# Kernel optimization log

Measured on AMD Instinct MI355X. Metric: run time of the kernel, lower is better.

The kernel has to match this reference:

```python
import jax, jax.numpy as jnp
import numpy as np
from jax import lax

B, C_IN, T = 128, 9, 2048
HID, OUT = 128, 6
NEW_T = T // 4          # two MaxPool1d(2)
N = B * NEW_T           # 65536 graph nodes
E = 524288              # edges
FEAT = 32               # out-channels of 2nd conv


def setup_inputs() -> dict:
    key = jax.random.key(0)
    ks = jax.random.split(key, 13)
    def w(k, shape, fan_in):
        return (jax.random.normal(k, shape, jnp.float32) / np.sqrt(fan_in)).astype(jnp.float32)
    return {
        "x": jax.random.normal(ks[0], (B, C_IN, T), jnp.float32),
        "edge_index": jax.random.randint(ks[1], (2, E), 0, N, jnp.int32),
        "conv1_w": w(ks[2], (16, C_IN, 5), C_IN * 5),
        "conv1_b": jnp.zeros((16,), jnp.float32),
        "conv2_w": w(ks[3], (FEAT, 16, 5), 16 * 5),
        "conv2_b": jnp.zeros((FEAT,), jnp.float32),
        "gcn1_w": w(ks[4], (FEAT, HID), FEAT),
        "gcn1_b": jnp.zeros((HID,), jnp.float32),
        "gcn2_w": w(ks[5], (HID, HID), HID),
        "gcn2_b": jnp.zeros((HID,), jnp.float32),
        "cls_w": w(ks[6], (HID, OUT), HID),
        "cls_b": jnp.zeros((OUT,), jnp.float32),
    }


def _conv1d(x, w, b):
    # x: [B, C, T], w: [O, I, K] (OIH), 'same' padding for k=5
    y = lax.conv_general_dilated(x, w, window_strides=(1,), padding=[(2, 2)],
                                 dimension_numbers=("NCH", "OIH", "NCH"))
    return y + b[None, :, None]


def _maxpool2(x):
    return lax.reduce_window(x, -jnp.inf, lax.max, (1, 1, 2), (1, 1, 2), "VALID")


def _gcn(x, w, b, src, dst, deg_inv_sqrt):
    # PyG GCNConv: sym-normalized aggregation with self loops.
    xw = x @ w                                             # [N, F]
    norm = deg_inv_sqrt[src] * deg_inv_sqrt[dst]           # [E]
    msg = xw[src] * norm[:, None]                          # gather + scale
    agg = jax.ops.segment_sum(msg, dst, num_segments=N)    # scatter-add
    agg = agg + xw * (deg_inv_sqrt * deg_inv_sqrt)[:, None]  # self loops
    return agg + b


def reference(x, edge_index, conv1_w, conv1_b, conv2_w, conv2_b,
              gcn1_w, gcn1_b, gcn2_w, gcn2_b, cls_w, cls_b):
    # temporal conv stack
    h = _maxpool2(jax.nn.relu(_conv1d(x, conv1_w, conv1_b)))
    h = _maxpool2(jax.nn.relu(_conv1d(h, conv2_w, conv2_b)))   # [B, 32, NEW_T]
    nodes = jnp.transpose(h, (0, 2, 1)).reshape(-1, FEAT)       # [N, 32]

    src, dst = edge_index[0], edge_index[1]
    # degree at dst, +1 for self loop
    deg = jax.ops.segment_sum(jnp.ones((E,), jnp.float32), dst, num_segments=N) + 1.0
    deg_inv_sqrt = lax.rsqrt(deg)

    g = jax.nn.relu(_gcn(nodes, gcn1_w, gcn1_b, src, dst, deg_inv_sqrt))
    g = jax.nn.relu(_gcn(g, gcn2_w, gcn2_b, src, dst, deg_inv_sqrt))

    pooled = g.reshape(B, NEW_T, HID).mean(axis=1)              # [B, HID]
    return pooled @ cls_w + cls_b                               # [B, OUT]
```

## Files before the change

kernel.cpp:

```cpp
#include <hip/hip_runtime.h>
#include <hip/hip_bf16.h>

#define BB    128
#define C_IN  9
#define T0    2048
#define T1    1024
#define T2    512
#define NN    65536
#define EE    524288
#define FEAT  32
#define HID   128
#define OUTC  6
#define CAP   64

typedef __attribute__((ext_vector_type(8))) short bf16x8;
typedef __attribute__((ext_vector_type(4))) float f32x4;

__device__ __forceinline__ float bf_lo(unsigned u) { return __uint_as_float(u << 16); }
__device__ __forceinline__ float bf_hi(unsigned u) { return __uint_as_float(u & 0xffff0000u); }
__device__ __forceinline__ unsigned short f2bf(float f) {
    unsigned x = __float_as_uint(f);
    return (unsigned short)((x + 0x7fffu + ((x >> 16) & 1u)) >> 16);
}
__device__ __forceinline__ float disv(int deg) { return rsqrtf((float)deg + 1.0f); }

__global__ __launch_bounds__(256) void k_zw(int4* __restrict__ cnt4,
                                            const float* __restrict__ w2,
                                            unsigned short* __restrict__ wt2) {
    int gid = blockIdx.x * 256 + threadIdx.x;
    cnt4[gid] = make_int4(0, 0, 0, 0);
    int col = gid & 127, k = gid >> 7;
    wt2[col * 128 + k] = f2bf(w2[(size_t)k * 128 + col]);
}

__global__ __launch_bounds__(256) void k_fillB(const int* __restrict__ ei,
                                               int* __restrict__ cnt,
                                               int* __restrict__ bucket) {
    int e = blockIdx.x * 256 + threadIdx.x;
    if (e >= EE) return;
    int s = ei[e];
    int d = ei[EE + e];
    int pos = atomicAdd(&cnt[d], 1);
    if (pos < CAP) bucket[d * CAP + pos] = s;
}

__global__ __launch_bounds__(256) void k_conv12(const float* __restrict__ x,
                                                const float* __restrict__ w1c,
                                                const float* __restrict__ b1c,
                                                const float* __restrict__ w2c,
                                                const float* __restrict__ b2c,
                                                const int* __restrict__ cnt,
                                                unsigned short* __restrict__ nodes_b) {
    __shared__ float sx[C_IN][272];
    __shared__ float sh[16][136];
    __shared__ float swt1[45 * 16];
    __shared__ float swt2[80 * 32];
    int b   = blockIdx.x >> 3;
    int qt  = blockIdx.x & 7;
    int tid = threadIdx.x;
    int t1lo = qt * 128 - 2;
    int gxb  = 2 * t1lo - 2;

    const float* xb = x + (size_t)b * C_IN * T0;
    #pragma unroll
    for (int c = 0; c < C_IN; ++c)
        for (int i = tid; i < 268; i += 256) {
            int g = gxb + i;
            sx[c][i] = ((unsigned)g < T0) ? xb[c * T0 + g] : 0.f;
        }
    for (int idx = tid; idx < 720; idx += 256) {
        int o = idx & 15, ck = idx >> 4;
        swt1[ck * 16 + o] = w1c[o * 45 + ck];
    }
    for (int idx = tid; idx < 2560; idx += 256) {
        int o = idx & 31, ck = idx >> 5;
        swt2[ck * 32 + o] = w2c[o * 80 + ck];
    }
    __syncthreads();

    {
        int o = tid >> 4, sub = tid & 15;
        float A0[9], A1[9];
        #pragma unroll
        for (int ii = 0; ii < 9; ++ii) { A0[ii] = 0.f; A1[ii] = 0.f; }
        #pragma unroll
        for (int c = 0; c < C_IN; ++c) {
            float wt[5];
            #pragma unroll
            for (int k = 0; k < 5; ++k) wt[k] = swt1[(c * 5 + k) * 16 + o];
            #pragma unroll
            for (int ii = 0; ii < 9; ++ii) {
                int pos = sub + ii * 16;
                if (pos < 132) {
                    const float* sp = &sx[c][2 * pos];
                    float2 p0 = *(const float2*)(sp);
                    float2 p1 = *(const float2*)(sp + 2);
                    float2 p2 = *(const float2*)(sp + 4);
                    A0[ii] += wt[0]*p0.x + wt[1]*p0.y + wt[2]*p1.x + wt[3]*p1.y + wt[4]*p2.x;
                    A1[ii] += wt[0]*p0.y + wt[1]*p1.x + wt[2]*p1.y + wt[3]*p2.x + wt[4]*p2.y;
                }
            }
        }
        float bo = b1c[o];
        #pragma unroll
        for (int ii = 0; ii < 9; ++ii) {
            int pos = sub + ii * 16;
            if (pos < 132) {
                int t = t1lo + pos;
                float h = fmaxf(fmaxf(A0[ii], A1[ii]) + bo, 0.f);
                sh[o][pos] = ((unsigned)t < T1) ? h : 0.f;
            }
        }
    }
    __syncthreads();

    int lane = tid & 63;
    int wv   = tid >> 6;
    int o    = lane & 31;
    int slot = lane >> 5;
    int ttl0 = wv * 16 + slot * 8;

    float acc[16];
    #pragma unroll
    for (int i = 0; i < 16; ++i) acc[i] = 0.f;

    #pragma unroll
    for (int c = 0; c < 16; ++c) {
        float wt[5];
        #pragma unroll
        for (int k = 0; k < 5; ++k) wt[k] = swt2[(c * 5 + k) * 32 + o];
        #pragma unroll
        for (int cb = 0; cb < 2; ++cb) {
            int Pb = 2 * ttl0 + 8 * cb;
            float4 i0 = *(const float4*)&sh[c][Pb];
            float4 i1 = *(const float4*)&sh[c][Pb + 4];
            float4 i2 = *(const float4*)&sh[c][Pb + 8];
            float in[12] = {i0.x,i0.y,i0.z,i0.w, i1.x,i1.y,i1.z,i1.w, i2.x,i2.y,i2.z,i2.w};
            #pragma unroll
            for (int q = 0; q < 8; ++q) {
                float s = acc[cb * 8 + q];
                #pragma unroll
                for (int k = 0; k < 5; ++k) s += wt[k] * in[q + k];
                acc[cb * 8 + q] = s;
            }
        }
    }

    float bi = b2c[o];
    int node0 = b * T2 + qt * 64 + ttl0;
    size_t nbase = (size_t)node0 * FEAT + o;
    #pragma unroll
    for (int cb = 0; cb < 2; ++cb)
        #pragma unroll
        for (int jj = 0; jj < 4; ++jj) {
            int node = node0 + cb * 4 + jj;
            float v = fmaxf(fmaxf(acc[cb*8+2*jj], acc[cb*8+2*jj+1]) + bi, 0.f);
            nodes_b[nbase + (size_t)(cb * 4 + jj) * FEAT] = f2bf(v * disv(cnt[node]));
        }
}

__global__ __launch_bounds__(256) void k_gather1(const unsigned short* __restrict__ nodes_b,
                                                 const int* __restrict__ cnt,
                                                 const int* __restrict__ bucket,
                                                 float* __restrict__ aggN) {
    int t = blockIdx.x * 256 + threadIdx.x;
    int node = t >> 3;
    if (node >= NN) return;
    int lane = t & 7;
    int deg = cnt[node];
    const int* bk = bucket + node * CAP;
    const uint2* nb = (const uint2*)nodes_b;
    uint2 q = nb[(size_t)node * 8 + lane];
    float a0 = bf_lo(q.x), a1 = bf_hi(q.x), a2 = bf_lo(q.y), a3 = bf_hi(q.y);
    for (int j = 0; j < deg; ++j) {
        int s = bk[j];
        uint2 p = nb[(size_t)s * 8 + lane];
        a0 += bf_lo(p.x); a1 += bf_hi(p.x); a2 += bf_lo(p.y); a3 += bf_hi(p.y);
    }
    float dd = disv(deg);
    float4 r; r.x = a0 * dd; r.y = a1 * dd; r.z = a2 * dd; r.w = a3 * dd;
    ((float4*)aggN)[(size_t)node * 8 + lane] = r;
}

__global__ __launch_bounds__(256) void k_fused(const float* __restrict__ aggN,
                                               const float* __restrict__ w1,
                                               const unsigned short* __restrict__ wt2,
                                               const float* __restrict__ b1,
                                               const int* __restrict__ cnt,
                                               unsigned short* __restrict__ xws2) {
    __shared__ union {
        struct { float an[32][132]; float w1s[32][132]; } p1;
        short sa[128 * 128];
    } u;
    __shared__ short sW[128 * 128];

    int tid = threadIdx.x;
    int rowBase = blockIdx.x * 128;

    #pragma unroll
    for (int it = 0; it < 8; ++it) {
        int cr = it * 16 + (tid >> 4);
        int ck = tid & 15;
        uint4 v = *(const uint4*)(wt2 + cr * 128 + ck * 8);
        *(uint4*)&sW[cr * 128 + ((ck * 8) ^ ((cr & 7) << 3))] = v;
    }
    {
        int ar = tid & 127;
        int half = tid >> 7;
        const float* arow = aggN + (size_t)(rowBase + ar) * FEAT + half * 16;
        #pragma unroll
        for (int q = 0; q < 4; ++q) {
            float4 va = *(const float4*)(arow + q * 4);
            int kb = half * 16 + q * 4;
            u.p1.an[kb + 0][ar] = va.x;
            u.p1.an[kb + 1][ar] = va.y;
            u.p1.an[kb + 2][ar] = va.z;
            u.p1.an[kb + 3][ar] = va.w;
        }
        #pragma unroll
        for (int it = 0; it < 4; ++it) {
            int i = tid + it * 256;
            int k  = i >> 5;
            int c4 = (i & 31) * 4;
            *(float4*)&u.p1.w1s[k][c4] = *(const float4*)(w1 + k * HID + c4);
        }
    }
    __syncthreads();

    int tr = tid >> 4, tc = tid & 15;
    float acc[8][8];
    #pragma unroll
    for (int i = 0; i < 8; ++i)
        #pragma unroll
        for (int j = 0; j < 8; ++j) acc[i][j] = 0.f;

    #pragma unroll 8
    for (int k = 0; k < FEAT; ++k) {
        float4 a0 = *(const float4*)&u.p1.an[k][tr * 8];
        float4 a1 = *(const float4*)&u.p1.an[k][tr * 8 + 4];
        float4 b0 = *(const float4*)&u.p1.w1s[k][tc * 8];
        float4 b1v = *(const float4*)&u.p1.w1s[k][tc * 8 + 4];
        float av[8] = {a0.x, a0.y, a0.z, a0.w, a1.x, a1.y, a1.z, a1.w};
        float bv[8] = {b0.x, b0.y, b0.z, b0.w, b1v.x, b1v.y, b1v.z, b1v.w};
        #pragma unroll
        for (int i = 0; i < 8; ++i)
            #pragma unroll
            for (int j = 0; j < 8; ++j) acc[i][j] += av[i] * bv[j];
    }
    __syncthreads();

    {
        float4 bb0 = *(const float4*)(b1 + tc * 8);
        float4 bb1 = *(const float4*)(b1 + tc * 8 + 4);
        float bv[8] = {bb0.x, bb0.y, bb0.z, bb0.w, bb1.x, bb1.y, bb1.z, bb1.w};
        #pragma unroll
        for (int i = 0; i < 8; ++i) {
            int row = tr * 8 + i;
            unsigned short us[8];
            #pragma unroll
            for (int j = 0; j < 8; ++j) us[j] = f2bf(fmaxf(acc[i][j] + bv[j], 0.f));
            uint4 pv;
            pv.x = (unsigned)us[0] | ((unsigned)us[1] << 16);
            pv.y = (unsigned)us[2] | ((unsigned)us[3] << 16);
            pv.z = (unsigned)us[4] | ((unsigned)us[5] << 16);
            pv.w = (unsigned)us[6] | ((unsigned)us[7] << 16);
            *(uint4*)&u.sa[row * 128 + ((tc * 8) ^ ((row & 7) << 3))] = pv;
        }
    }
    __syncthreads();

    int lane = tid & 63;
    int wv   = tid >> 6;
    int lrow = lane & 15;
    int kg   = lane >> 4;

    f32x4 zero = {0.f, 0.f, 0.f, 0.f};
    f32x4 macc[2][8];
    #pragma unroll
    for (int rt = 0; rt < 2; ++rt)
        #pragma unroll
        for (int ct = 0; ct < 8; ++ct) macc[rt][ct] = zero;

    #pragma unroll
    for (int ks = 0; ks < 4; ++ks) {
        int kb8 = ks * 4 + kg;
        bf16x8 af[2];
        #pragma unroll
        for (int rt = 0; rt < 2; ++rt) {
            int r = wv * 32 + rt * 16 + lrow;
            af[rt] = *(const bf16x8*)&u.sa[r * 128 + ((kb8 * 8) ^ ((r & 7) << 3))];
        }
        #pragma unroll
        for (int ct = 0; ct < 8; ++ct) {
            int c = ct * 16 + lrow;
            bf16x8 bfr = *(const bf16x8*)&sW[c * 128 + ((kb8 * 8) ^ ((c & 7) << 3))];
            macc[0][ct] = __builtin_amdgcn_mfma_f32_16x16x32_bf16(af[0], bfr, macc[0][ct], 0, 0, 0);
            macc[1][ct] = __builtin_amdgcn_mfma_f32_16x16x32_bf16(af[1], bfr, macc[1][ct], 0, 0, 0);
        }
    }

    #pragma unroll
    for (int rt = 0; rt < 2; ++rt) {
        int r0 = rowBase + wv * 32 + rt * 16 + kg * 4;
        #pragma unroll
        for (int q = 0; q < 4; ++q) {
            int grow = r0 + q;
            float d = disv(cnt[grow]);
            unsigned short* op = xws2 + (size_t)grow * HID + lrow;
            #pragma unroll
            for (int ct = 0; ct < 8; ++ct)
                op[ct * 16] = f2bf(macc[rt][ct][q] * d);
        }
    }
}

__global__ __launch_bounds__(256) void k_gather2(const unsigned short* __restrict__ xws2,
                                                 const int* __restrict__ cnt,
                                                 const int* __restrict__ bucket,
                                                 const float* __restrict__ b2,
                                                 float* __restrict__ partial) {
    __shared__ float sred[16][136];
    int t = blockIdx.x * 256 + threadIdx.x;
    int node = t >> 4;
    int lane = t & 15;
    int nloc = threadIdx.x >> 4;
    int deg = cnt[node];
    const int* bk = bucket + node * CAP;
    const uint4* xv = (const uint4*)xws2;
    uint4 q = xv[(size_t)node * 16 + lane];
    float a0 = bf_lo(q.x), a1 = bf_hi(q.x), a2 = bf_lo(q.y), a3 = bf_hi(q.y);
    float a4 = bf_lo(q.z), a5 = bf_hi(q.z), a6 = bf_lo(q.w), a7 = bf_hi(q.w);
    for (int j = 0; j < deg; ++j) {
        int s = bk[j];
        uint4 p = xv[(size_t)s * 16 + lane];
        a0 += bf_lo(p.x); a1 += bf_hi(p.x); a2 += bf_lo(p.y); a3 += bf_hi(p.y);
        a4 += bf_lo(p.z); a5 += bf_hi(p.z); a6 += bf_lo(p.w); a7 += bf_hi(p.w);
    }
    float dd = disv(deg);
    float4 pb0 = *(const float4*)(b2 + lane * 8);
    float4 pb1 = *(const float4*)(b2 + lane * 8 + 4);
    float* sp = &sred[nloc][lane * 8];
    sp[0] = fmaxf(a0 * dd + pb0.x, 0.f);
    sp[1] = fmaxf(a1 * dd + pb0.y, 0.f);
    sp[2] = fmaxf(a2 * dd + pb0.z, 0.f);
    sp[3] = fmaxf(a3 * dd + pb0.w, 0.f);
    sp[4] = fmaxf(a4 * dd + pb1.x, 0.f);
    sp[5] = fmaxf(a5 * dd + pb1.y, 0.f);
    sp[6] = fmaxf(a6 * dd + pb1.z, 0.f);
    sp[7] = fmaxf(a7 * dd + pb1.w, 0.f);
    __syncthreads();
    int f = threadIdx.x;
    if (f < 128) {
        float s = 0.f;
        #pragma unroll
        for (int n = 0; n < 16; ++n) s += sred[n][f];
        partial[(size_t)blockIdx.x * HID + f] = s;
    }
}

__global__ __launch_bounds__(128) void k_cls(const float* __restrict__ partial,
                                             const float* __restrict__ clsw,
                                             const float* __restrict__ clsb,
                                             float* __restrict__ out) {
    __shared__ float pooled[HID];
    int b = blockIdx.x;
    int f = threadIdx.x;
    const float* p = partial + (size_t)b * 32 * HID + f;
    float s = 0.f;
    #pragma unroll 8
    for (int c = 0; c < 32; ++c) s += p[c * HID];
    pooled[f] = s;
    __syncthreads();
    if (f < OUTC) {
        float acc = 0.f;
        #pragma unroll 8
        for (int k = 0; k < HID; ++k) acc += pooled[k] * clsw[k * OUTC + f];
        out[b * OUTC + f] = acc * (1.0f / (float)T2) + clsb[f];
    }
}

extern "C" void kernel_launch(void* const* d_in, const int* in_sizes, int n_in,
                              void* d_out, int out_size, void* d_ws, size_t ws_size,
                              hipStream_t stream) {
    const float* x    = (const float*)d_in[0];
    const int*   ei   = (const int*)d_in[1];
    const float* c1w  = (const float*)d_in[2];
    const float* c1b  = (const float*)d_in[3];
    const float* c2w  = (const float*)d_in[4];
    const float* c2b  = (const float*)d_in[5];
    const float* g1w  = (const float*)d_in[6];
    const float* g1b  = (const float*)d_in[7];
    const float* g2w  = (const float*)d_in[8];
    const float* g2b  = (const float*)d_in[9];
    const float* clsw = (const float*)d_in[10];
    const float* clsb = (const float*)d_in[11];
    float* out = (float*)d_out;

    float* ws = (float*)d_ws;
    float* aggN     = ws;
    float* partial  = ws + 2097152;
    unsigned short* wt2 = (unsigned short*)(ws + 2621440);
    unsigned short* nodes_b = (unsigned short*)(ws + 2629632);
    unsigned short* xws2 = (unsigned short*)(ws + 3678208);
    int* cnt        = (int*)(ws + 7872512);
    int* bucket     = (int*)(ws + 7938048);

    k_zw   <<<64, 256, 0, stream>>>((int4*)cnt, g2w, wt2);
    k_fillB<<<EE / 256, 256, 0, stream>>>(ei, cnt, bucket);

    k_conv12<<<BB * 8, 256, 0, stream>>>(x, c1w, c1b, c2w, c2b, cnt, nodes_b);

    k_gather1<<<(NN * 8) / 256, 256, 0, stream>>>(nodes_b, cnt, bucket, aggN);

    k_fused<<<NN / 128, 256, 0, stream>>>(aggN, g1w, wt2, g1b, cnt, xws2);

    k_gather2<<<(NN * 16) / 256, 256, 0, stream>>>(xws2, cnt, bucket, g2b, partial);

    k_cls<<<BB, 128, 0, stream>>>(partial, clsw, clsb, out);
}
```

Baseline: 141.1 us.

## Store gathered layer-1 aggregates in bf16 and shrink fused GEMM tile to 64 rows

The layer-1 gather now writes its normalized aggregates as packed bf16 instead of fp32, which halves the intermediate traffic between the gather and the fused GEMM kernel. The fused kernel processes 64 rows per block instead of 128. It drops the shared-memory copy of the second weight matrix and reads MFMA B fragments straight from global memory, which cuts LDS use so more blocks can be resident. In exchange the kernel now issues repeated global/L2 weight reads and loses some precision on the aggregates. It also leaves two dead uint2 loads (v0, v1) in the staging code.

```diff
diff --git a/kernel.cpp b/kernel.cpp
--- a/kernel.cpp
+++ b/kernel.cpp
@@ -162,7 +162,7 @@
 __global__ __launch_bounds__(256) void k_gather1(const unsigned short* __restrict__ nodes_b,
                                                  const int* __restrict__ cnt,
                                                  const int* __restrict__ bucket,
-                                                 float* __restrict__ aggN) {
+                                                 unsigned int* __restrict__ aggN_b) {
     int t = blockIdx.x * 256 + threadIdx.x;
     int node = t >> 3;
     if (node >= NN) return;
@@ -178,45 +178,39 @@
         a0 += bf_lo(p.x); a1 += bf_hi(p.x); a2 += bf_lo(p.y); a3 += bf_hi(p.y);
     }
     float dd = disv(deg);
-    float4 r; r.x = a0 * dd; r.y = a1 * dd; r.z = a2 * dd; r.w = a3 * dd;
-    ((float4*)aggN)[(size_t)node * 8 + lane] = r;
-}
-
-__global__ __launch_bounds__(256) void k_fused(const float* __restrict__ aggN,
+    uint2 r;
+    r.x = (unsigned)f2bf(a0 * dd) | ((unsigned)f2bf(a1 * dd) << 16);
+    r.y = (unsigned)f2bf(a2 * dd) | ((unsigned)f2bf(a3 * dd) << 16);
+    ((uint2*)aggN_b)[(size_t)node * 8 + lane] = r;
+}
+
+__global__ __launch_bounds__(256) void k_fused(const unsigned int* __restrict__ aggN_b,
                                                const float* __restrict__ w1,
                                                const unsigned short* __restrict__ wt2,
                                                const float* __restrict__ b1,
                                                const int* __restrict__ cnt,
                                                unsigned short* __restrict__ xws2) {
     __shared__ union {
-        struct { float an[32][132]; float w1s[32][132]; } p1;
-        short sa[128 * 128];
+        struct { float an[32][68]; float w1s[32][132]; } p1;
+        short sa[64 * 128];
     } u;
-    __shared__ short sW[128 * 128];
 
     int tid = threadIdx.x;
-    int rowBase = blockIdx.x * 128;
-
-    #pragma unroll
-    for (int it = 0; it < 8; ++it) {
-        int cr = it * 16 + (tid >> 4);
-        int ck = tid & 15;
-        uint4 v = *(const uint4*)(wt2 + cr * 128 + ck * 8);
-        *(uint4*)&sW[cr * 128 + ((ck * 8) ^ ((cr & 7) << 3))] = v;
-    }
+    int rowBase = blockIdx.x * 64;
+
     {
-        int ar = tid & 127;
-        int half = tid >> 7;
-        const float* arow = aggN + (size_t)(rowBase + ar) * FEAT + half * 16;
-        #pragma unroll
-        for (int q = 0; q < 4; ++q) {
-            float4 va = *(const float4*)(arow + q * 4);
-            int kb = half * 16 + q * 4;
-            u.p1.an[kb + 0][ar] = va.x;
-            u.p1.an[kb + 1][ar] = va.y;
-            u.p1.an[kb + 2][ar] = va.z;
-            u.p1.an[kb + 3][ar] = va.w;
-        }
+        int row = tid >> 2;
+        int qq  = tid & 3;
+        uint2 v0 = *(const uint2*)(aggN_b + (size_t)(rowBase + row) * 8 + qq * 2);
+        uint2 v1 = *(const uint2*)(aggN_b + (size_t)(rowBase + row) * 8 + qq * 2 + 1);
+        const unsigned* ap = aggN_b + (size_t)(rowBase + row) * 16 + qq * 4;
+        unsigned w0 = ap[0], w1u = ap[1], w2u = ap[2], w3 = ap[3];
+        int k0 = qq * 8;
+        u.p1.an[k0 + 0][row] = bf_lo(w0); u.p1.an[k0 + 1][row] = bf_hi(w0);
+        u.p1.an[k0 + 2][row] = bf_lo(w1u); u.p1.an[k0 + 3][row] = bf_hi(w1u);
+        u.p1.an[k0 + 4][row] = bf_lo(w2u); u.p1.an[k0 + 5][row] = bf_hi(w2u);
+        u.p1.an[k0 + 6][row] = bf_lo(w3); u.p1.an[k0 + 7][row] = bf_hi(w3);
+        (void)v0; (void)v1;
         #pragma unroll
         for (int it = 0; it < 4; ++it) {
             int i = tid + it * 256;
@@ -228,22 +222,21 @@
     __syncthreads();
 
     int tr = tid >> 4, tc = tid & 15;
-    float acc[8][8];
-    #pragma unroll
-    for (int i = 0; i < 8; ++i)
+    float acc[4][8];
+    #pragma unroll
+    for (int i = 0; i < 4; ++i)
         #pragma unroll
         for (int j = 0; j < 8; ++j) acc[i][j] = 0.f;
 
     #pragma unroll 8
     for (int k = 0; k < FEAT; ++k) {
-        float4 a0 = *(const float4*)&u.p1.an[k][tr * 8];
-        float4 a1 = *(const float4*)&u.p1.an[k][tr * 8 + 4];
+        float4 a0 = *(const float4*)&u.p1.an[k][tr * 4];
         float4 b0 = *(const float4*)&u.p1.w1s[k][tc * 8];
         float4 b1v = *(const float4*)&u.p1.w1s[k][tc * 8 + 4];
-        float av[8] = {a0.x, a0.y, a0.z, a0.w, a1.x, a1.y, a1.z, a1.w};
+        float av[4] = {a0.x, a0.y, a0.z, a0.w};
         float bv[8] = {b0.x, b0.y, b0.z, b0.w, b1v.x, b1v.y, b1v.z, b1v.w};
         #pragma unroll
-        for (int i = 0; i < 8; ++i)
+        for (int i = 0; i < 4; ++i)
             #pragma unroll
             for (int j = 0; j < 8; ++j) acc[i][j] += av[i] * bv[j];
     }
@@ -254,8 +247,8 @@
         float4 bb1 = *(const float4*)(b1 + tc * 8 + 4);
         float bv[8] = {bb0.x, bb0.y, bb0.z, bb0.w, bb1.x, bb1.y, bb1.z, bb1.w};
         #pragma unroll
-        for (int i = 0; i < 8; ++i) {
-            int row = tr * 8 + i;
+        for (int i = 0; i < 4; ++i) {
+            int row = tr * 4 + i;
             unsigned short us[8];
             #pragma unroll
             for (int j = 0; j < 8; ++j) us[j] = f2bf(fmaxf(acc[i][j] + bv[j], 0.f));
@@ -275,42 +268,32 @@
     int kg   = lane >> 4;
 
     f32x4 zero = {0.f, 0.f, 0.f, 0.f};
-    f32x4 macc[2][8];
-    #pragma unroll
-    for (int rt = 0; rt < 2; ++rt)
-        #pragma unroll
-        for (int ct = 0; ct < 8; ++ct) macc[rt][ct] = zero;
-
+    f32x4 macc[8];
+    #pragma unroll
+    for (int ct = 0; ct < 8; ++ct) macc[ct] = zero;
+
+    int r = wv * 16 + lrow;
     #pragma unroll
     for (int ks = 0; ks < 4; ++ks) {
         int kb8 = ks * 4 + kg;
-        bf16x8 af[2];
-        #pragma unroll
-        for (int rt = 0; rt < 2; ++rt) {
-            int r = wv * 32 + rt * 16 + lrow;
-            af[rt] = *(const bf16x8*)&u.sa[r * 128 + ((kb8 * 8) ^ ((r & 7) << 3))];
-        }
+        bf16x8 af = *(const bf16x8*)&u.sa[r * 128 + ((kb8 * 8) ^ ((r & 7) << 3))];
         #pragma unroll
         for (int ct = 0; ct < 8; ++ct) {
             int c = ct * 16 + lrow;
-            bf16x8 bfr = *(const bf16x8*)&sW[c * 128 + ((kb8 * 8) ^ ((c & 7) << 3))];
-            macc[0][ct] = __builtin_amdgcn_mfma_f32_16x16x32_bf16(af[0], bfr, macc[0][ct], 0, 0, 0);
-            macc[1][ct] = __builtin_amdgcn_mfma_f32_16x16x32_bf16(af[1], bfr, macc[1][ct], 0, 0, 0);
-        }
-    }
-
-    #pragma unroll
-    for (int rt = 0; rt < 2; ++rt) {
-        int r0 = rowBase + wv * 32 + rt * 16 + kg * 4;
-        #pragma unroll
-        for (int q = 0; q < 4; ++q) {
-            int grow = r0 + q;
-            float d = disv(cnt[grow]);
-            unsigned short* op = xws2 + (size_t)grow * HID + lrow;
-            #pragma unroll
-            for (int ct = 0; ct < 8; ++ct)
-                op[ct * 16] = f2bf(macc[rt][ct][q] * d);
-        }
+            bf16x8 bfr = *(const bf16x8*)(wt2 + (size_t)c * 128 + kb8 * 8);
+            macc[ct] = __builtin_amdgcn_mfma_f32_16x16x32_bf16(af, bfr, macc[ct], 0, 0, 0);
+        }
+    }
+
+    int r0 = rowBase + wv * 16 + kg * 4;
+    #pragma unroll
+    for (int q = 0; q < 4; ++q) {
+        int grow = r0 + q;
+        float d = disv(cnt[grow]);
+        unsigned short* op = xws2 + (size_t)grow * HID + lrow;
+        #pragma unroll
+        for (int ct = 0; ct < 8; ++ct)
+            op[ct * 16] = f2bf(macc[ct][q] * d);
     }
 }
 
@@ -397,22 +380,22 @@
     float* out = (float*)d_out;
 
     float* ws = (float*)d_ws;
-    float* aggN     = ws;
-    float* partial  = ws + 2097152;
-    unsigned short* wt2 = (unsigned short*)(ws + 2621440);
-    unsigned short* nodes_b = (unsigned short*)(ws + 2629632);
-    unsigned short* xws2 = (unsigned short*)(ws + 3678208);
-    int* cnt        = (int*)(ws + 7872512);
-    int* bucket     = (int*)(ws + 7938048);
+    unsigned int* aggN_b = (unsigned int*)ws;
+    float* partial  = ws + 1048576;
+    unsigned short* wt2 = (unsigned short*)(ws + 1572864);
+    unsigned short* nodes_b = (unsigned short*)(ws + 1581056);
+    unsigned short* xws2 = (unsigned short*)(ws + 2629632);
+    int* cnt        = (int*)(ws + 6823936);
+    int* bucket     = (int*)(ws + 6889472);
 
     k_zw   <<<64, 256, 0, stream>>>((int4*)cnt, g2w, wt2);
     k_fillB<<<EE / 256, 256, 0, stream>>>(ei, cnt, bucket);
 
     k_conv12<<<BB * 8, 256, 0, stream>>>(x, c1w, c1b, c2w, c2b, cnt, nodes_b);
 
-    k_gather1<<<(NN * 8) / 256, 256, 0, stream>>>(nodes_b, cnt, bucket, aggN);
-
-    k_fused<<<NN / 128, 256, 0, stream>>>(aggN, g1w, wt2, g1b, cnt, xws2);
+    k_gather1<<<(NN * 8) / 256, 256, 0, stream>>>(nodes_b, cnt, bucket, aggN_b);
+
+    k_fused<<<NN / 64, 256, 0, stream>>>(aggN_b, g1w, wt2, g1b, cnt, xws2);
 
     k_gather2<<<(NN * 16) / 256, 256, 0, stream>>>(xws2, cnt, bucket, g2b, partial);
 
```

Result: slower. 153.6 us (+8.8%).
